# Optimization experiments

Measured on AMD Instinct MI355X. Metric: run time of the kernel, lower is better.

## Reference

```python
import math
import jax, jax.numpy as jnp
import numpy as np

EMBED_SIZE = 1024
NUM_HEADS = 16
HEAD_DIM = EMBED_SIZE // NUM_HEADS
N, L = 8, 1024
MASK_FILL = -1e3  # value used by masked_fill in the original (NOT -inf)
SCALE = 1.0 / math.sqrt(EMBED_SIZE)  # original divides by embed_size**0.5, not head_dim


def setup_inputs() -> dict:
    key = jax.random.key(0)
    ks = jax.random.split(key, 7)
    values = jax.random.normal(ks[0], (N, L, EMBED_SIZE), dtype=jnp.float32)
    keys_t = jax.random.normal(ks[1], (N, L, EMBED_SIZE), dtype=jnp.float32)
    queries = jax.random.normal(ks[2], (N, L, EMBED_SIZE), dtype=jnp.float32)
    attn_mask = jax.random.randint(ks[3], (1, 1, L, L), 0, 2, dtype=jnp.int32)
    scr_key_padding_mask = jax.random.randint(ks[4], (N, 1, 1, L), 0, 2, dtype=jnp.int32)
    # fc_out: nn.Linear(embed_size, embed_size) with bias
    fc_w = jax.random.normal(ks[5], (EMBED_SIZE, EMBED_SIZE), dtype=jnp.float32) * (1.0 / math.sqrt(EMBED_SIZE))
    fc_b = jax.random.normal(ks[6], (EMBED_SIZE,), dtype=jnp.float32) * 0.01
    return {"values": values, "keys": keys_t, "queries": queries,
            "fc_w": fc_w, "fc_b": fc_b,
            "attn_mask": attn_mask, "scr_key_padding_mask": scr_key_padding_mask}


def reference(values, keys, queries, fc_w, fc_b, attn_mask, scr_key_padding_mask):
    n, q_len, e = queries.shape
    k_len = keys.shape[1]
    h, d = NUM_HEADS, HEAD_DIM
    # NOTE: the original defines per-head Linear projections but never applies them
    v = values.reshape(n, k_len, h, d)
    k = keys.reshape(n, k_len, h, d)
    q = queries.reshape(n, q_len, h, d)
    energy = jnp.einsum('nqhd,nkhd->nhqk', q, k)  # [n, h, q, k]
    am = attn_mask[:, :, :k_len, :k_len]
    energy = jnp.where(am == 0, MASK_FILL, energy)
    energy = jnp.where(scr_key_padding_mask == 0, MASK_FILL, energy)
    attention = jax.nn.softmax(energy * SCALE, axis=3)
    out = jnp.einsum('nhql,nlhd->nqhd', attention, v).reshape(n, q_len, h * d)
    return out @ fc_w.T + fc_b
```

## Files before the change

### kernel.cpp

```cpp
#include <hip/hip_runtime.h>

#define L_SEQ 1024
#define EMB 1024
#define NH 16
#define HD 64

typedef _Float16 half8 __attribute__((ext_vector_type(8)));
typedef _Float16 half4v __attribute__((ext_vector_type(4)));
typedef __fp16 h2 __attribute__((ext_vector_type(2)));
typedef float f32x4 __attribute__((ext_vector_type(4)));
typedef float f32x16 __attribute__((ext_vector_type(16)));
typedef float fvec4 __attribute__((ext_vector_type(4)));
typedef unsigned int u32;
typedef u32 u32x4 __attribute__((ext_vector_type(4)));
typedef unsigned long long u64;

constexpr float C2 = 0.045084220027780106f;

constexpr int FP = 40;
constexpr int PP = 72;

__device__ __forceinline__ void async16(const void* g, void* l) {
    __builtin_amdgcn_global_load_lds((const __attribute__((address_space(1))) u32*)g,
                                     (__attribute__((address_space(3))) u32*)l, 16, 0, 0);
}

__global__ void pack_mask_kernel(const int* __restrict__ am, u32* __restrict__ bits,
                                 const int* __restrict__ pad, u32* __restrict__ pbits) {
    const int i = blockIdx.x * 256 + threadIdx.x;
    const int lane = threadIdx.x & 63;
    u64 b = __ballot(am[i] != 0);
    if (lane == 0)       bits[i >> 5] = (u32)b;
    else if (lane == 32) bits[i >> 5] = (u32)(b >> 32);
    if (blockIdx.x < 32) {
        const int j = blockIdx.x * 256 + threadIdx.x;
        u64 pb = __ballot(pad[j] != 0);
        if (lane == 0)       pbits[j >> 5] = (u32)pb;
        else if (lane == 32) pbits[j >> 5] = (u32)(pb >> 32);
    }
}

__global__ void convert_w_kernel(const float* __restrict__ w, _Float16* __restrict__ o) {
    size_t i = ((size_t)blockIdx.x * blockDim.x + threadIdx.x) * 4;
    fvec4 v = *(const fvec4*)(w + i);
    half4v h;
#pragma unroll
    for (int j = 0; j < 4; ++j) h[j] = (_Float16)v[j];
    *(half4v*)(o + i) = h;
}

__global__ __launch_bounds__(256) void cvt_kv_kernel(
    const float* __restrict__ keys, const float* __restrict__ values,
    _Float16* __restrict__ K16, _Float16* __restrict__ Vt16)
{
    __shared__ __align__(16) _Float16 Vt[64 * PP];
    const int tid = threadIdx.x;
    const int kt = blockIdx.x, h = blockIdx.y, n = blockIdx.z;
    const int kbase = kt * 64;
    const int r = tid >> 2, c0 = (tid & 3) * 16;
    const int nh = n * NH + h;

    {
        const float* src = keys + ((size_t)(n * L_SEQ + kbase + r)) * EMB + h * HD + c0;
        fvec4 a0 = *(const fvec4*)(src),     a1 = *(const fvec4*)(src + 4);
        fvec4 a2 = *(const fvec4*)(src + 8), a3 = *(const fvec4*)(src + 12);
        half8 o0, o1;
#pragma unroll
        for (int j = 0; j < 4; ++j) {
            o0[j] = (_Float16)(a0[j] * C2); o0[j + 4] = (_Float16)(a1[j] * C2);
            o1[j] = (_Float16)(a2[j] * C2); o1[j + 4] = (_Float16)(a3[j] * C2);
        }
        _Float16* dst = K16 + ((size_t)nh * L_SEQ + kbase + r) * HD + c0;
        *(half8*)dst = o0; *(half8*)(dst + 8) = o1;
    }
    {
        const float* src = values + ((size_t)(n * L_SEQ + kbase + r)) * EMB + h * HD + c0;
        fvec4 vv[4];
        vv[0] = *(const fvec4*)(src);     vv[1] = *(const fvec4*)(src + 4);
        vv[2] = *(const fvec4*)(src + 8); vv[3] = *(const fvec4*)(src + 12);
#pragma unroll
        for (int i = 0; i < 16; ++i)
            Vt[(c0 + i) * PP + r] = (_Float16)vv[i >> 2][i & 3];
    }
    __syncthreads();
    {
        const int d = tid >> 2, k0 = (tid & 3) * 16;
        half8 v0 = *(const half8*)(&Vt[d * PP + k0]);
        half8 v1 = *(const half8*)(&Vt[d * PP + k0 + 8]);
        _Float16* dst = Vt16 + ((size_t)nh * HD + d) * L_SEQ + kbase + k0;
        *(half8*)dst = v0; *(half8*)(dst + 8) = v1;
    }
}

__global__ __launch_bounds__(256, 3) void attn_kernel(
    const _Float16* __restrict__ K16, const _Float16* __restrict__ Vt16,
    const float* __restrict__ queries, const u32* __restrict__ mbits,
    const u32* __restrict__ pbits, _Float16* __restrict__ out_f16)
{
    __shared__ __align__(16) _Float16 K_lds[2][64 * 64];
    __shared__ __align__(16) _Float16 V_lds[2][64 * 64];
    __shared__ __align__(8)  u32 mtab[32];

    const int tid  = threadIdx.x;
    const int lane = tid & 63;
    const int wv   = tid >> 6;
    const int l32  = lane & 31;
    const int hi   = lane >> 5;
    const int bid  = blockIdx.x;
    const int nh = bid & 127, qt = bid >> 7;
    const int n = nh >> 4, h = nh & 15;
    const int qbase = qt * 128;
    const int q = qbase + wv * 32 + l32;
    const int rsw = l32 & 7;

    const _Float16* Kt_base = K16 + (size_t)nh * L_SEQ * HD;
    const _Float16* Vt_base = Vt16 + (size_t)nh * HD * L_SEQ;
    const int gch = (lane & 7) ^ ((lane >> 3) & 7);

    auto stage = [&](int buf, int kt) {
        const int kbase = kt * 64;
#pragma unroll
        for (int s2 = 0; s2 < 2; ++s2) {
            const int row = wv * 16 + s2 * 8 + (lane >> 3);
            async16(Kt_base + (size_t)(kbase + row) * HD + gch * 8,
                    &K_lds[buf][(wv * 16 + s2 * 8) * 64]);
            async16(Vt_base + (size_t)row * L_SEQ + kbase + gch * 8,
                    &V_lds[buf][(wv * 16 + s2 * 8) * 64]);
        }
    };

    stage(0, 0);

    if (tid < 16) {
        mtab[tid * 2]     = ((tid & 1) ? 0x3C00u : 0u) | ((tid & 2) ? 0x3C000000u : 0u);
        mtab[tid * 2 + 1] = ((tid & 4) ? 0x3C00u : 0u) | ((tid & 8) ? 0x3C000000u : 0u);
    }

    half8 qf[4];
    {
        const float* qp = queries + ((size_t)(n * L_SEQ + q)) * EMB + h * HD;
#pragma unroll
        for (int c = 0; c < 4; ++c) {
            fvec4 a = *(const fvec4*)(qp + c * 16 + hi * 8);
            fvec4 b = *(const fvec4*)(qp + c * 16 + hi * 8 + 4);
#pragma unroll
            for (int j = 0; j < 4; ++j) { qf[c][j] = (_Float16)a[j]; qf[c][j + 4] = (_Float16)b[j]; }
        }
    }

    f32x16 Ov[2];
#pragma unroll
    for (int dt = 0; dt < 2; ++dt)
#pragma unroll
        for (int r = 0; r < 16; ++r) Ov[dt][r] = 0.f;
    float lsum = 0.f;
    const h2 one2 = {(__fp16)1.f, (__fp16)1.f};

    int cur = 0;
#pragma unroll 2
    for (int kt = 0; kt < L_SEQ / 64; ++kt) {
        __syncthreads();
        if (kt + 1 < L_SEQ / 64) stage(cur ^ 1, kt + 1);

        const uint2 wmq = *(const uint2*)(&mbits[(size_t)q * 32 + kt * 2]);
        u32 w[2];
        w[0] = wmq.x & pbits[(n << 5) + (kt << 1)];
        w[1] = wmq.y & pbits[(n << 5) + (kt << 1) + 1];

        f32x16 St[2];
#pragma unroll
        for (int i = 0; i < 2; ++i)
#pragma unroll
            for (int r = 0; r < 16; ++r) St[i][r] = 0.f;

        const _Float16* kb = &K_lds[cur][0];
        __builtin_amdgcn_s_setprio(1);
#pragma unroll
        for (int c = 0; c < 4; ++c) {
            const int ch = ((2 * c + hi) ^ rsw) * 8;
            half8 kf0 = *(const half8*)(kb + l32 * 64 + ch);
            half8 kf1 = *(const half8*)(kb + (32 + l32) * 64 + ch);
            St[0] = __builtin_amdgcn_mfma_f32_32x32x16_f16(kf0, qf[c], St[0], 0, 0, 0);
            St[1] = __builtin_amdgcn_mfma_f32_32x32x16_f16(kf1, qf[c], St[1], 0, 0, 0);
        }
        __builtin_amdgcn_s_setprio(0);

        u32 pa[4][4];
#pragma unroll
        for (int i = 0; i < 2; ++i) {
#pragma unroll
            for (int rgp = 0; rgp < 2; ++rgp) {
                const int rg_a = 2 * rgp, rg_b = 2 * rgp + 1;
                const u32 m4a = (w[i] >> (8 * rg_a + 4 * hi)) & 15u;
                const u32 m4b = (w[i] >> (8 * rg_b + 4 * hi)) & 15u;
                const uint2 mma = *(const uint2*)(&mtab[m4a * 2]);
                const uint2 mmb = *(const uint2*)(&mtab[m4b * 2]);
                const float pa0 = __builtin_amdgcn_exp2f(St[i][4 * rg_a + 0]);
                const float pa1 = __builtin_amdgcn_exp2f(St[i][4 * rg_a + 1]);
                const float pa2 = __builtin_amdgcn_exp2f(St[i][4 * rg_a + 2]);
                const float pa3 = __builtin_amdgcn_exp2f(St[i][4 * rg_a + 3]);
                const float pb0 = __builtin_amdgcn_exp2f(St[i][4 * rg_b + 0]);
                const float pb1 = __builtin_amdgcn_exp2f(St[i][4 * rg_b + 1]);
                const float pb2 = __builtin_amdgcn_exp2f(St[i][4 * rg_b + 2]);
                const float pb3 = __builtin_amdgcn_exp2f(St[i][4 * rg_b + 3]);
                const h2 a0 = __builtin_amdgcn_cvt_pkrtz(pa0, pa1) * __builtin_bit_cast(h2, mma.x);
                const h2 a1 = __builtin_amdgcn_cvt_pkrtz(pa2, pa3) * __builtin_bit_cast(h2, mma.y);
                const h2 b0 = __builtin_amdgcn_cvt_pkrtz(pb0, pb1) * __builtin_bit_cast(h2, mmb.x);
                const h2 b1 = __builtin_amdgcn_cvt_pkrtz(pb2, pb3) * __builtin_bit_cast(h2, mmb.y);
                lsum = __builtin_amdgcn_fdot2(a0, one2, lsum, false);
                lsum = __builtin_amdgcn_fdot2(a1, one2, lsum, false);
                lsum = __builtin_amdgcn_fdot2(b0, one2, lsum, false);
                lsum = __builtin_amdgcn_fdot2(b1, one2, lsum, false);
                u32 A0 = __builtin_bit_cast(u32, a0), A1 = __builtin_bit_cast(u32, a1);
                u32 B0 = __builtin_bit_cast(u32, b0), B1 = __builtin_bit_cast(u32, b1);
                asm("v_permlane32_swap_b32 %0, %1" : "+v"(A0), "+v"(B0));
                asm("v_permlane32_swap_b32 %0, %1" : "+v"(A1), "+v"(B1));
                const int ks = i * 2 + rgp;
                pa[ks][0] = A0; pa[ks][1] = A1; pa[ks][2] = B0; pa[ks][3] = B1;
            }
        }

        const _Float16* vb = &V_lds[cur][0];
        __builtin_amdgcn_s_setprio(1);
#pragma unroll
        for (int ks = 0; ks < 4; ++ks) {
            u32x4 pw = {pa[ks][0], pa[ks][1], pa[ks][2], pa[ks][3]};
            half8 pB = __builtin_bit_cast(half8, pw);
            const int ch = ((2 * ks + hi) ^ rsw) * 8;
            half8 vf0 = *(const half8*)(vb + l32 * 64 + ch);
            half8 vf1 = *(const half8*)(vb + (32 + l32) * 64 + ch);
            Ov[0] = __builtin_amdgcn_mfma_f32_32x32x16_f16(pB, vf0, Ov[0], 0, 0, 0);
            Ov[1] = __builtin_amdgcn_mfma_f32_32x32x16_f16(pB, vf1, Ov[1], 0, 0, 0);
        }
        __builtin_amdgcn_s_setprio(0);
        cur ^= 1;
    }

    lsum += __shfl_xor(lsum, 32);
    float linv[16];
#pragma unroll
    for (int reg = 0; reg < 16; ++reg) {
        const int qrel = (reg & 3) + 8 * (reg >> 2) + 4 * hi;
        linv[reg] = 1.0f / fmaxf(__shfl(lsum, qrel), 1e-25f);
    }
#pragma unroll
    for (int reg = 0; reg < 16; ++reg) {
        const int qrow = qbase + wv * 32 + (reg & 3) + 8 * (reg >> 2) + 4 * hi;
        _Float16* op = out_f16 + ((size_t)(n * L_SEQ + qrow)) * EMB + h * HD;
        op[l32]      = (_Float16)(Ov[0][reg] * linv[reg]);
        op[32 + l32] = (_Float16)(Ov[1][reg] * linv[reg]);
    }
}

__global__ __launch_bounds__(256) void fc_kernel(
    const _Float16* __restrict__ A, const _Float16* __restrict__ W,
    const float* __restrict__ bias, float* __restrict__ C)
{
    __shared__ __align__(16) _Float16 As[128 * FP];
    __shared__ __align__(16) _Float16 Ws[128 * FP];

    const int tid = threadIdx.x;
    const int lane = tid & 63;
    const int wv = tid >> 6;
    const int l16 = lane & 15;
    const int quad = lane >> 4;
    const int wm = (wv >> 1) * 64, wn = (wv & 1) * 64;
    const int Mb = blockIdx.x * 128, Nb = blockIdx.y * 128;

    f32x4 acc[4][4];
#pragma unroll
    for (int i = 0; i < 4; ++i)
#pragma unroll
        for (int j = 0; j < 4; ++j) acc[i][j] = (f32x4){0.f, 0.f, 0.f, 0.f};

    for (int k0 = 0; k0 < EMB; k0 += 32) {
        __syncthreads();
#pragma unroll
        for (int s = 0; s < 2; ++s) {
            const int id = tid + s * 256;
            const int row = id >> 2, ch = (id & 3) * 8;
            *(half8*)(&As[row * FP + ch]) = *(const half8*)(A + (size_t)(Mb + row) * EMB + k0 + ch);
            *(half8*)(&Ws[row * FP + ch]) = *(const half8*)(W + (size_t)(Nb + row) * EMB + k0 + ch);
        }
        __syncthreads();

        half8 af[4], bf[4];
#pragma unroll
        for (int i = 0; i < 4; ++i) {
            af[i] = *(const half8*)(&As[(wm + i * 16 + l16) * FP + quad * 8]);
            bf[i] = *(const half8*)(&Ws[(wn + i * 16 + l16) * FP + quad * 8]);
        }
#pragma unroll
        for (int i = 0; i < 4; ++i)
#pragma unroll
            for (int j = 0; j < 4; ++j)
                acc[i][j] = __builtin_amdgcn_mfma_f32_16x16x32_f16(af[i], bf[j], acc[i][j], 0, 0, 0);
    }

#pragma unroll
    for (int i = 0; i < 4; ++i) {
        const int m = Mb + wm + i * 16 + quad * 4;
#pragma unroll
        for (int j = 0; j < 4; ++j) {
            const int jc = Nb + wn + j * 16 + l16;
            const float b = bias[jc];
#pragma unroll
            for (int reg = 0; reg < 4; ++reg)
                C[(size_t)(m + reg) * EMB + jc] = acc[i][j][reg] + b;
        }
    }
}

extern "C" void kernel_launch(void* const* d_in, const int* in_sizes, int n_in,
                              void* d_out, int out_size, void* d_ws, size_t ws_size,
                              hipStream_t stream) {
    const float* values  = (const float*)d_in[0];
    const float* keys    = (const float*)d_in[1];
    const float* queries = (const float*)d_in[2];
    const float* fc_w    = (const float*)d_in[3];
    const float* fc_b    = (const float*)d_in[4];
    const int*   amask   = (const int*)d_in[5];
    const int*   pmask   = (const int*)d_in[6];
    float* out = (float*)d_out;

    char* w = (char*)d_ws;
    _Float16* attn_out = (_Float16*)w;
    _Float16* w_f16    = (_Float16*)(w + (size_t)16 * 1024 * 1024);
    u32*      mbits    = (u32*)(w + (size_t)18 * 1024 * 1024);
    u32*      pbits    = (u32*)(w + (size_t)18 * 1024 * 1024 + 128 * 1024);
    _Float16* K16      = (_Float16*)(w + (size_t)19 * 1024 * 1024);
    _Float16* Vt16     = (_Float16*)(w + (size_t)35 * 1024 * 1024);

    pack_mask_kernel<<<4096, 256, 0, stream>>>(amask, mbits, pmask, pbits);
    convert_w_kernel<<<1024, 256, 0, stream>>>(fc_w, w_f16);
    cvt_kv_kernel<<<dim3(16, 16, 8), 256, 0, stream>>>(keys, values, K16, Vt16);
    attn_kernel<<<1024, 256, 0, stream>>>(K16, Vt16, queries, mbits, pbits, attn_out);
    fc_kernel<<<dim3(64, 8), 256, 0, stream>>>(attn_out, w_f16, fc_b, out);
}
```

Before: 237.2 us.

## Double-buffer FC GEMM with async LDS loads and prefetch attention mask bits

The output-projection GEMM now stages A and W tiles straight into LDS with async global-to-LDS loads. It uses two buffers, an XOR-swizzled layout and a K-step of 64, so the next tile loads while MFMAs run on the current one and one barrier per step is removed. The attention kernel also prefetches the next tile's packed mask and padding bits one iteration ahead, hiding their global load latency. This doubles FC shared memory use, which may reduce occupancy.

```diff
diff --git a/kernel.cpp b/kernel.cpp
--- a/kernel.cpp
+++ b/kernel.cpp
@@ -17,7 +17,6 @@
 
 constexpr float C2 = 0.045084220027780106f;
 
-constexpr int FP = 40;
 constexpr int PP = 72;
 
 __device__ __forceinline__ void async16(const void* g, void* l) {
@@ -129,6 +128,9 @@
         }
     };
 
+    uint2 wm_cur = *(const uint2*)(&mbits[(size_t)q * 32]);
+    u32 pl_cur = pbits[n << 5];
+    u32 ph_cur = pbits[(n << 5) + 1];
     stage(0, 0);
 
     if (tid < 16) {
@@ -160,12 +162,19 @@
 #pragma unroll 2
     for (int kt = 0; kt < L_SEQ / 64; ++kt) {
         __syncthreads();
-        if (kt + 1 < L_SEQ / 64) stage(cur ^ 1, kt + 1);
-
-        const uint2 wmq = *(const uint2*)(&mbits[(size_t)q * 32 + kt * 2]);
+
+        uint2 wm_next = {0u, 0u};
+        u32 pl_next = 0u, ph_next = 0u;
+        if (kt + 1 < L_SEQ / 64) {
+            wm_next = *(const uint2*)(&mbits[(size_t)q * 32 + (kt + 1) * 2]);
+            pl_next = pbits[(n << 5) + ((kt + 1) << 1)];
+            ph_next = pbits[(n << 5) + ((kt + 1) << 1) + 1];
+            stage(cur ^ 1, kt + 1);
+        }
+
         u32 w[2];
-        w[0] = wmq.x & pbits[(n << 5) + (kt << 1)];
-        w[1] = wmq.y & pbits[(n << 5) + (kt << 1) + 1];
+        w[0] = wm_cur.x & pl_cur;
+        w[1] = wm_cur.y & ph_cur;
 
         f32x16 St[2];
 #pragma unroll
@@ -233,6 +242,8 @@
             Ov[1] = __builtin_amdgcn_mfma_f32_32x32x16_f16(pB, vf1, Ov[1], 0, 0, 0);
         }
         __builtin_amdgcn_s_setprio(0);
+
+        wm_cur = wm_next; pl_cur = pl_next; ph_cur = ph_next;
         cur ^= 1;
     }
 
@@ -256,8 +267,8 @@
     const _Float16* __restrict__ A, const _Float16* __restrict__ W,
     const float* __restrict__ bias, float* __restrict__ C)
 {
-    __shared__ __align__(16) _Float16 As[128 * FP];
-    __shared__ __align__(16) _Float16 Ws[128 * FP];
+    __shared__ __align__(16) _Float16 As[2][128 * 64];
+    __shared__ __align__(16) _Float16 Ws[2][128 * 64];
 
     const int tid = threadIdx.x;
     const int lane = tid & 63;
@@ -266,6 +277,17 @@
     const int quad = lane >> 4;
     const int wm = (wv >> 1) * 64, wn = (wv & 1) * 64;
     const int Mb = blockIdx.x * 128, Nb = blockIdx.y * 128;
+    const int xr = l16 & 7;
+
+    auto stage = [&](int buf, int k0) {
+#pragma unroll
+        for (int s = 0; s < 4; ++s) {
+            const int row = wv * 32 + s * 8 + (lane >> 3);
+            const int sc = (lane & 7) ^ (row & 7);
+            async16(A + (size_t)(Mb + row) * EMB + k0 + sc * 8, &As[buf][(wv * 32 + s * 8) * 64]);
+            async16(W + (size_t)(Nb + row) * EMB + k0 + sc * 8, &Ws[buf][(wv * 32 + s * 8) * 64]);
+        }
+    };
 
     f32x4 acc[4][4];
 #pragma unroll
@@ -273,28 +295,32 @@
 #pragma unroll
         for (int j = 0; j < 4; ++j) acc[i][j] = (f32x4){0.f, 0.f, 0.f, 0.f};
 
-    for (int k0 = 0; k0 < EMB; k0 += 32) {
+    stage(0, 0);
+    int cur = 0;
+#pragma unroll 2
+    for (int k0 = 0; k0 < EMB; k0 += 64) {
         __syncthreads();
-#pragma unroll
-        for (int s = 0; s < 2; ++s) {
-            const int id = tid + s * 256;
-            const int row = id >> 2, ch = (id & 3) * 8;
-            *(half8*)(&As[row * FP + ch]) = *(const half8*)(A + (size_t)(Mb + row) * EMB + k0 + ch);
-            *(half8*)(&Ws[row * FP + ch]) = *(const half8*)(W + (size_t)(Nb + row) * EMB + k0 + ch);
-        }
-        __syncthreads();
-
-        half8 af[4], bf[4];
-#pragma unroll
-        for (int i = 0; i < 4; ++i) {
-            af[i] = *(const half8*)(&As[(wm + i * 16 + l16) * FP + quad * 8]);
-            bf[i] = *(const half8*)(&Ws[(wn + i * 16 + l16) * FP + quad * 8]);
-        }
+        if (k0 + 64 < EMB) stage(cur ^ 1, k0 + 64);
+
+        half8 af[4][2], bf[4][2];
 #pragma unroll
         for (int i = 0; i < 4; ++i)
 #pragma unroll
+            for (int kk = 0; kk < 2; ++kk) {
+                const int ch = (((kk * 4 + quad) ^ xr)) * 8;
+                af[i][kk] = *(const half8*)(&As[cur][(wm + i * 16 + l16) * 64 + ch]);
+                bf[i][kk] = *(const half8*)(&Ws[cur][(wn + i * 16 + l16) * 64 + ch]);
+            }
+        __builtin_amdgcn_s_setprio(1);
+#pragma unroll
+        for (int i = 0; i < 4; ++i)
+#pragma unroll
             for (int j = 0; j < 4; ++j)
-                acc[i][j] = __builtin_amdgcn_mfma_f32_16x16x32_f16(af[i], bf[j], acc[i][j], 0, 0, 0);
+#pragma unroll
+                for (int kk = 0; kk < 2; ++kk)
+                    acc[i][j] = __builtin_amdgcn_mfma_f32_16x16x32_f16(af[i][kk], bf[j][kk], acc[i][j], 0, 0, 0);
+        __builtin_amdgcn_s_setprio(0);
+        cur ^= 1;
     }
 
 #pragma unroll
```

Result: faster. 224.8 us (-5.2%).
